# Performance work log

Hardware: AMD Instinct MI355X
Metric: run time of the kernel (lower is better)

Reference implementation:

```python
import jax, jax.numpy as jnp
import numpy as np

EPS = 1e-5

def layer_norm(x, g, b):
    m = jnp.mean(x, axis=-1, keepdims=True)
    v = jnp.var(x, axis=-1, keepdims=True)
    return (x - m) * jax.lax.rsqrt(v + EPS) * g + b

def setup_inputs() -> dict:
    key = jax.random.key(0)
    ks = jax.random.split(key, 16)
    B, N, C_Z, C_H = 1, 512, 128, 128
    s_z = 1.0 / np.sqrt(C_Z)
    s_h = 1.0 / np.sqrt(C_H)
    inp = {
        "z": jax.random.normal(ks[0], (B, N, N, C_Z), jnp.float32),
        "mask": jnp.ones((B, N, N), jnp.float32),
        # linear weights stored as [in, out] so forward is x @ W + b
        "w_ag": jax.random.uniform(ks[1], (C_Z, C_H), jnp.float32, -s_z, s_z),
        "b_ag": jnp.zeros((C_H,), jnp.float32),
        "w_ap": jax.random.uniform(ks[2], (C_Z, C_H), jnp.float32, -s_z, s_z),
        "b_ap": jnp.zeros((C_H,), jnp.float32),
        "w_bg": jax.random.uniform(ks[3], (C_Z, C_H), jnp.float32, -s_z, s_z),
        "b_bg": jnp.zeros((C_H,), jnp.float32),
        "w_bp": jax.random.uniform(ks[4], (C_Z, C_H), jnp.float32, -s_z, s_z),
        "b_bp": jnp.zeros((C_H,), jnp.float32),
        "w_g": jax.random.uniform(ks[5], (C_Z, C_Z), jnp.float32, -s_z, s_z),
        "b_g": jnp.zeros((C_Z,), jnp.float32),
        "w_z": jax.random.uniform(ks[6], (C_H, C_Z), jnp.float32, -s_h, s_h),
        "b_z": jnp.zeros((C_Z,), jnp.float32),
        "ln_in_g": jnp.ones((C_Z,), jnp.float32),
        "ln_in_b": jnp.zeros((C_Z,), jnp.float32),
        "ln_out_g": jnp.ones((C_H,), jnp.float32),
        "ln_out_b": jnp.zeros((C_H,), jnp.float32),
    }
    return inp

def reference(z, mask, w_ag, b_ag, w_ap, b_ap, w_bg, b_bg, w_bp, b_bp,
              w_g, b_g, w_z, b_z, ln_in_g, ln_in_b, ln_out_g, ln_out_b):
    m = mask[..., None]                      # [B,N,N,1]
    zn = layer_norm(z, ln_in_g, ln_in_b)     # [B,N,N,Cz]
    a = m * jax.nn.sigmoid(zn @ w_ag + b_ag) * (zn @ w_ap + b_ap)  # [B,N,N,Ch]
    b = m * jax.nn.sigmoid(zn @ w_bg + b_bg) * (zn @ w_bp + b_bp)  # [B,N,N,Ch]
    # outgoing: p[i,j,c] = sum_k a[i,k,c] * b[j,k,c]
    x = jnp.einsum('bikc,bjkc->bijc', a, b)
    x = layer_norm(x, ln_out_g, ln_out_b)
    x = x @ w_z + b_z
    g = jax.nn.sigmoid(zn @ w_g + b_g)
    return x * g
```

## Files before the change

### kernel.cpp

```cpp
#include <hip/hip_runtime.h>
#include <hip/hip_bf16.h>
#include <math.h>


#define N 512
#define C 128
#define NN (N*N)
#define PK 136
#define PT 40
#define PX 137
#define ST 72

typedef __attribute__((ext_vector_type(8))) short bf16x8;
typedef __attribute__((ext_vector_type(4))) float f32x4;
typedef unsigned short u16;
typedef unsigned int u32;

__device__ __forceinline__ u16 f2bf(float f) {
    u32 u = __builtin_bit_cast(u32, f);
    u = (u + 0x7fffu + ((u >> 16) & 1u)) >> 16;
    return (u16)u;
}
__device__ __forceinline__ float bf2f(u16 h) {
    return __builtin_bit_cast(float, ((u32)h) << 16);
}
__device__ __forceinline__ float sigmoidf(float x) {
    return 1.f / (1.f + __expf(-x));
}

__global__ __launch_bounds__(256) void k_wt_all(
    const float* __restrict__ w0, const float* __restrict__ w1,
    const float* __restrict__ w2, const float* __restrict__ w3,
    const float* __restrict__ w4, const float* __restrict__ w5,
    const float* __restrict__ gin, const float* __restrict__ gout,
    u16* __restrict__ o0, u16* __restrict__ o1, u16* __restrict__ o2,
    u16* __restrict__ o3, u16* __restrict__ o4, u16* __restrict__ o5) {
    int sel = blockIdx.x >> 6;
    int idx = (blockIdx.x & 63) * 256 + threadIdx.x;
    const float* w = sel == 0 ? w0 : sel == 1 ? w1 : sel == 2 ? w2
                   : sel == 3 ? w3 : sel == 4 ? w4 : w5;
    u16* o = sel == 0 ? o0 : sel == 1 ? o1 : sel == 2 ? o2
           : sel == 3 ? o3 : sel == 4 ? o4 : o5;
    const float* g = (sel == 5) ? gout : gin;
    int co = idx >> 7, k = idx & 127;
    o[idx] = f2bf(g[k] * w[k * C + co]);
}

__global__ __launch_bounds__(256) void k_bias(
    const float* __restrict__ w0, const float* __restrict__ w1,
    const float* __restrict__ w2, const float* __restrict__ w3,
    const float* __restrict__ w4, const float* __restrict__ w5,
    const float* __restrict__ b0, const float* __restrict__ b1,
    const float* __restrict__ b2, const float* __restrict__ b3,
    const float* __restrict__ b4, const float* __restrict__ b5,
    const float* __restrict__ vin, const float* __restrict__ vout,
    float* __restrict__ obias) {
    int id = blockIdx.x * 256 + threadIdx.x;
    int m = id >> 7, cc = id & 127;
    const float* w = m == 0 ? w0 : m == 1 ? w1 : m == 2 ? w2
                   : m == 3 ? w3 : m == 4 ? w4 : w5;
    const float* b = m == 0 ? b0 : m == 1 ? b1 : m == 2 ? b2
                   : m == 3 ? b3 : m == 4 ? b4 : b5;
    const float* v = (m == 5) ? vout : vin;
    float acc = 0.f;
#pragma unroll 4
    for (int k = 0; k < 128; ++k) acc += v[k] * w[k * C + cc];
    obias[id] = b[cc] + acc;
}

__global__ __launch_bounds__(256) void k_proj_fused(
    const float* __restrict__ z, const float* __restrict__ mask,
    const u16* __restrict__ wag, const u16* __restrict__ wap,
    const u16* __restrict__ wbg, const u16* __restrict__ wbp,
    const u16* __restrict__ wgg, const float* __restrict__ biasAll,
    u16* __restrict__ aT, u16* __restrict__ bT, u16* __restrict__ gate) {
    __shared__ u16 sA[64 * PK];
    __shared__ u16 sT[4][16 * ST];
    long r0 = (long)blockIdx.x * 64;
    int tid = threadIdx.x, wave = tid >> 6, lane = tid & 63;
    int lo = lane & 15, quad = lane >> 4;

    {
        int rl = lane >> 2, cb = lane & 3;
        int row = wave * 16 + rl;
        const float* zr = z + (r0 + row) * C + cb * 32;
        float4 v[8];
        float s = 0.f, s2 = 0.f;
#pragma unroll
        for (int i = 0; i < 8; ++i) {
            v[i] = *(const float4*)(zr + i * 4);
            s  += v[i].x + v[i].y + v[i].z + v[i].w;
            s2 += v[i].x * v[i].x + v[i].y * v[i].y + v[i].z * v[i].z + v[i].w * v[i].w;
        }
        s += __shfl_xor(s, 1); s2 += __shfl_xor(s2, 1);
        s += __shfl_xor(s, 2); s2 += __shfl_xor(s2, 2);
        float mean = s * (1.f / 128.f);
        float rs = rsqrtf(s2 * (1.f / 128.f) - mean * mean + 1e-5f);
        u16* dst = &sA[row * PK + cb * 32];
#pragma unroll
        for (int j = 0; j < 4; ++j) {
            uint4 pk;
            pk.x = (u32)f2bf((v[2*j].x   - mean) * rs) | ((u32)f2bf((v[2*j].y   - mean) * rs) << 16);
            pk.y = (u32)f2bf((v[2*j].z   - mean) * rs) | ((u32)f2bf((v[2*j].w   - mean) * rs) << 16);
            pk.z = (u32)f2bf((v[2*j+1].x - mean) * rs) | ((u32)f2bf((v[2*j+1].y - mean) * rs) << 16);
            pk.w = (u32)f2bf((v[2*j+1].z - mean) * rs) | ((u32)f2bf((v[2*j+1].w - mean) * rs) << 16);
            *(uint4*)(dst + 8 * j) = pk;
        }
    }
    __syncthreads();

    int c0 = wave * 32;
    float msk[4][4];
#pragma unroll
    for (int mi = 0; mi < 4; ++mi)
#pragma unroll
        for (int r = 0; r < 4; ++r)
            msk[mi][r] = mask[r0 + mi * 16 + quad * 4 + r];

    u16* sTw = &sT[wave][0];

    auto pair_stage = [&](const u16* __restrict__ wG, const float* __restrict__ bG,
                          const u16* __restrict__ wP, const float* __restrict__ bP,
                          u16* __restrict__ outT) {
#pragma unroll
        for (int nt = 0; nt < 2; ++nt) {
            int c = c0 + nt * 16 + lo;
            bf16x8 fG[4], fP[4];
#pragma unroll
            for (int ki = 0; ki < 4; ++ki) {
                fG[ki] = *(const bf16x8*)(wG + c * C + ki * 32 + quad * 8);
                fP[ki] = *(const bf16x8*)(wP + c * C + ki * 32 + quad * 8);
            }
            f32x4 aG[4], aP[4];
#pragma unroll
            for (int mi = 0; mi < 4; ++mi) { aG[mi] = (f32x4)(0.f); aP[mi] = (f32x4)(0.f); }
#pragma unroll
            for (int mi = 0; mi < 4; ++mi)
#pragma unroll
                for (int ki = 0; ki < 4; ++ki) {
                    bf16x8 av = *(const bf16x8*)(&sA[(mi * 16 + lo) * PK + ki * 32 + quad * 8]);
                    aG[mi] = __builtin_amdgcn_mfma_f32_16x16x32_bf16(av, fG[ki], aG[mi], 0, 0, 0);
                    aP[mi] = __builtin_amdgcn_mfma_f32_16x16x32_bf16(av, fP[ki], aP[mi], 0, 0, 0);
                }
            float bGv = bG[c], bPv = bP[c];
#pragma unroll
            for (int mi = 0; mi < 4; ++mi) {
                float v0 = msk[mi][0] * sigmoidf(aG[mi][0] + bGv) * (aP[mi][0] + bPv);
                float v1 = msk[mi][1] * sigmoidf(aG[mi][1] + bGv) * (aP[mi][1] + bPv);
                float v2 = msk[mi][2] * sigmoidf(aG[mi][2] + bGv) * (aP[mi][2] + bPv);
                float v3 = msk[mi][3] * sigmoidf(aG[mi][3] + bGv) * (aP[mi][3] + bPv);
                uint2 pk;
                pk.x = (u32)f2bf(v0) | ((u32)f2bf(v1) << 16);
                pk.y = (u32)f2bf(v2) | ((u32)f2bf(v3) << 16);
                *(uint2*)(&sTw[lo * ST + mi * 16 + quad * 4]) = pk;
            }
            {
                int cl = lane >> 2, pr = lane & 3;
                uint4 x0 = *(const uint4*)(&sTw[cl * ST + pr * 16]);
                uint4 x1 = *(const uint4*)(&sTw[cl * ST + pr * 16 + 8]);
                u16* g = outT + (long)(c0 + nt * 16 + cl) * NN + r0 + pr * 16;
                *(uint4*)(g) = x0;
                *(uint4*)(g + 8) = x1;
            }
        }
    };
    pair_stage(wag, biasAll + 0,   wap, biasAll + 128, aT);
    pair_stage(wbg, biasAll + 256, wbp, biasAll + 384, bT);

    {
        f32x4 gA[2][4];
#pragma unroll
        for (int nt = 0; nt < 2; ++nt) {
            bf16x8 gF[4];
#pragma unroll
            for (int ki = 0; ki < 4; ++ki)
                gF[ki] = *(const bf16x8*)(wgg + (c0 + nt * 16 + lo) * C + ki * 32 + quad * 8);
#pragma unroll
            for (int mi = 0; mi < 4; ++mi) gA[nt][mi] = (f32x4)(0.f);
#pragma unroll
            for (int mi = 0; mi < 4; ++mi)
#pragma unroll
                for (int ki = 0; ki < 4; ++ki) {
                    bf16x8 av = *(const bf16x8*)(&sA[(mi * 16 + lo) * PK + ki * 32 + quad * 8]);
                    gA[nt][mi] = __builtin_amdgcn_mfma_f32_16x16x32_bf16(av, gF[ki], gA[nt][mi], 0, 0, 0);
                }
        }
        __syncthreads();
        const float* bg5 = biasAll + 512;
#pragma unroll
        for (int nt = 0; nt < 2; ++nt) {
            int c = c0 + nt * 16 + lo;
            float bv = bg5[c];
#pragma unroll
            for (int mi = 0; mi < 4; ++mi)
#pragma unroll
                for (int r = 0; r < 4; ++r)
                    sA[(mi * 16 + quad * 4 + r) * PK + c] = f2bf(sigmoidf(gA[nt][mi][r] + bv));
        }
        __syncthreads();
#pragma unroll
        for (int p = 0; p < 4; ++p) {
            int linear = p * 2048 + tid * 8;
            int row = linear >> 7, k = linear & 127;
            *(uint4*)(gate + (r0 + row) * C + k) = *(const uint4*)(&sA[row * PK + k]);
        }
    }
}

__global__ __launch_bounds__(256) void k_tri(const u16* __restrict__ aT,
                                             const u16* __restrict__ bT,
                                             u16* __restrict__ xT) {
    __shared__ u16 sA[128 * PT];
    __shared__ u16 sB[128 * PT];
    int bid = blockIdx.x;
    int swz = (bid & 7) * 256 + (bid >> 3);
    int c = swz >> 4;
    int i0 = ((swz >> 2) & 3) * 128, j0 = (swz & 3) * 128;
    const u16* aBase = aT + (long)c * NN + (long)i0 * N;
    const u16* bBase = bT + (long)c * NN + (long)j0 * N;
    int tid = threadIdx.x;
    int wave = tid >> 6, lane = tid & 63, lo = lane & 15, quad = lane >> 4;
    int mq = (wave >> 1) * 64, nq = (wave & 1) * 64;
    f32x4 acc[4][4];
#pragma unroll
    for (int mi = 0; mi < 4; ++mi)
#pragma unroll
        for (int ni = 0; ni < 4; ++ni) acc[mi][ni] = (f32x4)(0.f);

    int srow[2], sk[2];
#pragma unroll
    for (int p = 0; p < 2; ++p) {
        int linear = p * 2048 + tid * 8;
        srow[p] = linear >> 5; sk[p] = linear & 31;
    }
    uint4 ra[2], rb[2];
#pragma unroll
    for (int p = 0; p < 2; ++p) {
        ra[p] = *(const uint4*)(aBase + srow[p] * N + sk[p]);
        rb[p] = *(const uint4*)(bBase + srow[p] * N + sk[p]);
    }
    for (int kk = 0; kk < N; kk += 32) {
        __syncthreads();
#pragma unroll
        for (int p = 0; p < 2; ++p) {
            *(uint4*)(&sA[srow[p] * PT + sk[p]]) = ra[p];
            *(uint4*)(&sB[srow[p] * PT + sk[p]]) = rb[p];
        }
        __syncthreads();
        if (kk + 32 < N) {
#pragma unroll
            for (int p = 0; p < 2; ++p) {
                ra[p] = *(const uint4*)(aBase + srow[p] * N + kk + 32 + sk[p]);
                rb[p] = *(const uint4*)(bBase + srow[p] * N + kk + 32 + sk[p]);
            }
        }
        bf16x8 af[4], bfr[4];
#pragma unroll
        for (int mi = 0; mi < 4; ++mi)
            af[mi] = *(const bf16x8*)(&sA[(mq + mi * 16 + lo) * PT + quad * 8]);
#pragma unroll
        for (int ni = 0; ni < 4; ++ni)
            bfr[ni] = *(const bf16x8*)(&sB[(nq + ni * 16 + lo) * PT + quad * 8]);
#pragma unroll
        for (int mi = 0; mi < 4; ++mi)
#pragma unroll
            for (int ni = 0; ni < 4; ++ni)
                acc[mi][ni] = __builtin_amdgcn_mfma_f32_16x16x32_bf16(af[mi], bfr[ni], acc[mi][ni], 0, 0, 0);
    }
    u16* outBase = xT + (long)c * NN;
#pragma unroll
    for (int mi = 0; mi < 4; ++mi)
#pragma unroll
        for (int ni = 0; ni < 4; ++ni)
#pragma unroll
            for (int r = 0; r < 4; ++r) {
                int gi = i0 + mq + mi * 16 + quad * 4 + r;
                int gj = j0 + nq + ni * 16 + lo;
                outBase[(long)gi * N + gj] = f2bf(acc[mi][ni][r]);
            }
}

__global__ __launch_bounds__(256) void k_out(
    const u16* __restrict__ xT, const u16* __restrict__ gate,
    const u16* __restrict__ wzT, const float* __restrict__ bz,
    float* __restrict__ out) {
    __shared__ float sX[64 * PX];
    __shared__ u16 sA[64 * PK];
    __shared__ float sRed[2][4][64];
    __shared__ float2 sMV[64];
    long r0 = (long)blockIdx.x * 64;
    int tid = threadIdx.x;
#pragma unroll
    for (int p = 0; p < 4; ++p) {
        int linear = p * 2048 + tid * 8;
        int cc = linear >> 6, jr = linear & 63;
        uint4 v = *(const uint4*)(xT + (long)cc * NN + r0 + jr);
        u16* u = (u16*)&v;
#pragma unroll
        for (int e = 0; e < 8; ++e) sX[(jr + e) * PX + cc] = bf2f(u[e]);
    }
    __syncthreads();
    {
        int jr = tid & 63, part = tid >> 6;
        float s = 0, s2 = 0;
#pragma unroll
        for (int c = part * 32; c < part * 32 + 32; ++c) {
            float v = sX[jr * PX + c];
            s += v; s2 += v * v;
        }
        sRed[0][part][jr] = s; sRed[1][part][jr] = s2;
    }
    __syncthreads();
    if (tid < 64) {
        float S = 0, S2 = 0;
#pragma unroll
        for (int p = 0; p < 4; ++p) { S += sRed[0][p][tid]; S2 += sRed[1][p][tid]; }
        float mean = S * (1.f / 128.f);
        float var = S2 * (1.f / 128.f) - mean * mean;
        sMV[tid] = make_float2(mean, rsqrtf(var + 1e-5f));
    }
    __syncthreads();
    {
        int row = tid & 63, c0 = (tid >> 6) * 32;
        float2 mv = sMV[row];
#pragma unroll
        for (int c = c0; c < c0 + 32; ++c)
            sA[row * PK + c] = f2bf((sX[row * PX + c] - mv.x) * mv.y);
    }
    __syncthreads();
    int wave = tid >> 6, lane = tid & 63, lo = lane & 15, quad = lane >> 4;
    int msub = wave * 16;
    bf16x8 av[4];
#pragma unroll
    for (int ki = 0; ki < 4; ++ki)
        av[ki] = *(const bf16x8*)(&sA[(msub + lo) * PK + ki * 32 + quad * 8]);
    f32x4 acc[8];
#pragma unroll
    for (int nt = 0; nt < 8; ++nt) acc[nt] = (f32x4)(0.f);
#pragma unroll
    for (int nt = 0; nt < 8; ++nt)
#pragma unroll
        for (int ki = 0; ki < 4; ++ki) {
            bf16x8 b8 = *(const bf16x8*)(wzT + (nt * 16 + lo) * C + ki * 32 + quad * 8);
            acc[nt] = __builtin_amdgcn_mfma_f32_16x16x32_bf16(av[ki], b8, acc[nt], 0, 0, 0);
        }
#pragma unroll
    for (int nt = 0; nt < 8; ++nt) {
        int c = nt * 16 + lo;
        float bzv = bz[c];
#pragma unroll
        for (int r = 0; r < 4; ++r) {
            int row = msub + quad * 4 + r;
            long rr = r0 + row;
            float g = bf2f(gate[rr * C + c]);
            out[rr * C + c] = (acc[nt][r] + bzv) * g;
        }
    }
}

extern "C" void kernel_launch(void* const* d_in, const int* in_sizes, int n_in,
                              void* d_out, int out_size, void* d_ws, size_t ws_size,
                              hipStream_t stream) {
    const float* z       = (const float*)d_in[0];
    const float* mask    = (const float*)d_in[1];
    const float* w_ag    = (const float*)d_in[2];
    const float* b_ag    = (const float*)d_in[3];
    const float* w_ap    = (const float*)d_in[4];
    const float* b_ap    = (const float*)d_in[5];
    const float* w_bg    = (const float*)d_in[6];
    const float* b_bg    = (const float*)d_in[7];
    const float* w_bp    = (const float*)d_in[8];
    const float* b_bp    = (const float*)d_in[9];
    const float* w_g     = (const float*)d_in[10];
    const float* b_g     = (const float*)d_in[11];
    const float* w_z     = (const float*)d_in[12];
    const float* b_z     = (const float*)d_in[13];
    const float* ln_in_g = (const float*)d_in[14];
    const float* ln_in_b = (const float*)d_in[15];
    const float* ln_out_g= (const float*)d_in[16];
    const float* ln_out_b= (const float*)d_in[17];
    float* out = (float*)d_out;

    char* ws = (char*)d_ws;
    u16* a_t  = (u16*)(ws);
    u16* b_t  = (u16*)(ws + 67108864L);
    u16* gate = (u16*)(ws + 134217728L);
    u16* x_t  = (u16*)(ws + 201326592L);
    u16* wag_t = (u16*)(ws + 268435456L);
    u16* wap_t = wag_t + 16384;
    u16* wbg_t = wag_t + 32768;
    u16* wbp_t = wag_t + 49152;
    u16* wg_t  = wag_t + 65536;
    u16* wz_t  = wag_t + 81920;
    float* biasAdj = (float*)(ws + 268435456L + 196608L);

    k_wt_all<<<384, 256, 0, stream>>>(w_ag, w_ap, w_bg, w_bp, w_g, w_z,
                                      ln_in_g, ln_out_g,
                                      wag_t, wap_t, wbg_t, wbp_t, wg_t, wz_t);

    k_bias<<<3, 256, 0, stream>>>(w_ag, w_ap, w_bg, w_bp, w_g, w_z,
                                  b_ag, b_ap, b_bg, b_bp, b_g, b_z,
                                  ln_in_b, ln_out_b, biasAdj);

    k_proj_fused<<<NN / 64, 256, 0, stream>>>(
        z, mask, wag_t, wap_t, wbg_t, wbp_t, wg_t, biasAdj,
        a_t, b_t, gate);

    k_tri<<<2048, 256, 0, stream>>>(a_t, b_t, x_t);

    k_out<<<NN / 64, 256, 0, stream>>>(x_t, gate, wz_t, biasAdj + 640, out);
}
```

Baseline: 669.8 us.

## Use direct global-to-LDS loads in triangle GEMM and drop register prefetch

Replaces the register-staged double-buffer prefetch in k_tri with global_load_lds 16-byte direct loads into unpadded LDS tiles. The grid becomes a 2D launch indexed by channel without the XCD swizzle. This cuts VGPR use and the LDS write instructions, at the cost of losing overlap of the next tile's global loads with the MFMA work. Unpadded 32-element rows may also raise LDS bank conflicts on the fragment reads.

New measurement: 579.3 us. 13.5% less time.

```diff
diff --git a/kernel.cpp b/kernel.cpp
--- a/kernel.cpp
+++ b/kernel.cpp
@@ -7,7 +7,6 @@
 #define C 128
 #define NN (N*N)
 #define PK 136
-#define PT 40
 #define PX 137
 #define ST 72
 
@@ -26,6 +25,11 @@
 }
 __device__ __forceinline__ float sigmoidf(float x) {
     return 1.f / (1.f + __expf(-x));
+}
+__device__ __forceinline__ void gload16(const u16* g, u16* lds) {
+    __builtin_amdgcn_global_load_lds(
+        (const __attribute__((address_space(1))) unsigned int*)g,
+        (__attribute__((address_space(3))) unsigned int*)lds, 16, 0, 0);
 }
 
 __global__ __launch_bounds__(256) void k_wt_all(
@@ -210,57 +214,39 @@
 __global__ __launch_bounds__(256) void k_tri(const u16* __restrict__ aT,
                                              const u16* __restrict__ bT,
                                              u16* __restrict__ xT) {
-    __shared__ u16 sA[128 * PT];
-    __shared__ u16 sB[128 * PT];
-    int bid = blockIdx.x;
-    int swz = (bid & 7) * 256 + (bid >> 3);
-    int c = swz >> 4;
-    int i0 = ((swz >> 2) & 3) * 128, j0 = (swz & 3) * 128;
+    __shared__ u16 sA[128 * 32];
+    __shared__ u16 sB[128 * 32];
+    int c = blockIdx.y;
+    int i0 = (blockIdx.x >> 2) * 128, j0 = (blockIdx.x & 3) * 128;
     const u16* aBase = aT + (long)c * NN + (long)i0 * N;
     const u16* bBase = bT + (long)c * NN + (long)j0 * N;
     int tid = threadIdx.x;
     int wave = tid >> 6, lane = tid & 63, lo = lane & 15, quad = lane >> 4;
     int mq = (wave >> 1) * 64, nq = (wave & 1) * 64;
+    int ld_row = lane >> 2;
+    int ld_col = (lane & 3) * 8;
     f32x4 acc[4][4];
 #pragma unroll
     for (int mi = 0; mi < 4; ++mi)
 #pragma unroll
         for (int ni = 0; ni < 4; ++ni) acc[mi][ni] = (f32x4)(0.f);
-
-    int srow[2], sk[2];
-#pragma unroll
-    for (int p = 0; p < 2; ++p) {
-        int linear = p * 2048 + tid * 8;
-        srow[p] = linear >> 5; sk[p] = linear & 31;
-    }
-    uint4 ra[2], rb[2];
-#pragma unroll
-    for (int p = 0; p < 2; ++p) {
-        ra[p] = *(const uint4*)(aBase + srow[p] * N + sk[p]);
-        rb[p] = *(const uint4*)(bBase + srow[p] * N + sk[p]);
-    }
     for (int kk = 0; kk < N; kk += 32) {
         __syncthreads();
 #pragma unroll
-        for (int p = 0; p < 2; ++p) {
-            *(uint4*)(&sA[srow[p] * PT + sk[p]]) = ra[p];
-            *(uint4*)(&sB[srow[p] * PT + sk[p]]) = rb[p];
+        for (int h = 0; h < 2; ++h) {
+            int ch = wave + h * 4;
+            int r = ch * 16 + ld_row;
+            gload16(aBase + (long)r * N + kk + ld_col, &sA[ch * 512]);
+            gload16(bBase + (long)r * N + kk + ld_col, &sB[ch * 512]);
         }
         __syncthreads();
-        if (kk + 32 < N) {
-#pragma unroll
-            for (int p = 0; p < 2; ++p) {
-                ra[p] = *(const uint4*)(aBase + srow[p] * N + kk + 32 + sk[p]);
-                rb[p] = *(const uint4*)(bBase + srow[p] * N + kk + 32 + sk[p]);
-            }
-        }
         bf16x8 af[4], bfr[4];
 #pragma unroll
         for (int mi = 0; mi < 4; ++mi)
-            af[mi] = *(const bf16x8*)(&sA[(mq + mi * 16 + lo) * PT + quad * 8]);
+            af[mi] = *(const bf16x8*)(&sA[(mq + mi * 16 + lo) * 32 + quad * 8]);
 #pragma unroll
         for (int ni = 0; ni < 4; ++ni)
-            bfr[ni] = *(const bf16x8*)(&sB[(nq + ni * 16 + lo) * PT + quad * 8]);
+            bfr[ni] = *(const bf16x8*)(&sB[(nq + ni * 16 + lo) * 32 + quad * 8]);
 #pragma unroll
         for (int mi = 0; mi < 4; ++mi)
 #pragma unroll
@@ -406,7 +392,7 @@
         z, mask, wag_t, wap_t, wbg_t, wbp_t, wg_t, biasAdj,
         a_t, b_t, gate);
 
-    k_tri<<<2048, 256, 0, stream>>>(a_t, b_t, x_t);
+    k_tri<<<dim3(16, 128), 256, 0, stream>>>(a_t, b_t, x_t);
 
     k_out<<<NN / 64, 256, 0, stream>>>(x_t, gate, wz_t, biasAdj + 640, out);
 }
```
